# Kernel tuning notes

Measured on AMD Instinct MI355X. Metric: run time of the kernel, lower is better.

Reference implementation:

```python
import jax, jax.numpy as jnp
import numpy as np

B, L, D, E, H = 4, 2048, 512, 8, 1024

def setup_inputs() -> dict:
    key = jax.random.key(0)
    k1, k2, k3, k4 = jax.random.split(key, 4)
    x = jax.random.normal(k1, (B, L, D), dtype=jnp.float32)
    weights = jax.random.uniform(k2, (B, L, E), dtype=jnp.float32)
    w1 = jax.random.normal(k3, (E, D, H), dtype=jnp.float32) * 0.02
    b1 = jnp.zeros((E, H), dtype=jnp.float32)
    w2 = jax.random.normal(k4, (E, H, D), dtype=jnp.float32) * 0.02
    b2 = jnp.zeros((E, D), dtype=jnp.float32)
    return {"x": x, "weights": weights, "w1": w1, "b1": b1, "w2": w2, "b2": b2}

def reference(x, weights, w1, b1, w2, b2):
    # h: [B, L, E, H]
    h = jnp.einsum('bld,edh->bleh', x, w1) + b1[None, None, :, :]
    h = jax.nn.gelu(h, approximate=False)  # torch F.gelu default is exact (erf)
    # out: [B, L, E, D]
    out = jnp.einsum('bleh,ehd->bled', h, w2) + b2[None, None, :, :]
    # weighted sum over experts -> [B, L, D]
    return jnp.einsum('bled,ble->bld', out, weights)
```

## Files before the change

kernel.cpp:

```cpp
#include <hip/hip_runtime.h>
#include <hip/hip_bf16.h>

#define DEV __device__ __forceinline__

typedef __bf16 bf16;
typedef __bf16 bf16x4 __attribute__((ext_vector_type(4)));
typedef __bf16 bf16x8 __attribute__((ext_vector_type(8)));
typedef float f32x4 __attribute__((ext_vector_type(4)));

static constexpr int Bb = 4, Ll = 2048, Dd = 512, Ee = 8, Hh = 1024;
static constexpr int Mm = Bb * Ll;
static constexpr int GKS = Ee * Hh;
static constexpr int TSZ = 65536;

DEV void gload_lds16(const void* g, void* l) {
  __builtin_amdgcn_global_load_lds(
      (const __attribute__((address_space(1))) unsigned int*)g,
      (__attribute__((address_space(3))) unsigned int*)l, 16, 0, 0);
}

DEV float gelu_fast(float h) {
  const float k = 0.7978845608028654f * 2.0f * 1.4426950408889634f;
  float h2 = h * h;
  float y = h * (k + (0.044715f * k) * h2);
  float t = exp2f(y);
  return h - h * __frcp_rn(t + 1.0f);
}

__global__ void cvt_x_kernel(const float* __restrict__ in, bf16* __restrict__ out, int n4) {
  int i = blockIdx.x * blockDim.x + threadIdx.x;
  if (i < n4) {
    float4 v = ((const float4*)in)[i];
    bf16x4 o = {(bf16)v.x, (bf16)v.y, (bf16)v.z, (bf16)v.w};
    ((bf16x4*)out)[i] = o;
  }
}

__global__ void transpose_cvt(const float* __restrict__ in, bf16* __restrict__ out,
                              int R, int C, size_t in_es, size_t out_es, int out_rs) {
  __shared__ float tile[64][65];
  const int e = blockIdx.z;
  const float* ip = in + (size_t)e * in_es;
  bf16* op = out + (size_t)e * out_es;
  const int r0 = blockIdx.y * 64, c0 = blockIdx.x * 64;
  const int tc = threadIdx.x & 63, tr = threadIdx.x >> 6;
#pragma unroll
  for (int i = 0; i < 16; ++i) {
    const int r = tr + i * 4;
    tile[r][tc] = ip[(size_t)(r0 + r) * C + c0 + tc];
  }
  __syncthreads();
  const int wr = threadIdx.x & 63, wc0 = threadIdx.x >> 6;
#pragma unroll
  for (int i = 0; i < 16; ++i) {
    const int c = wc0 + i * 4;
    op[(size_t)(c0 + c) * out_rs + r0 + wr] = (bf16)tile[wr][c];
  }
}

#define PIPE_DECLS                                                   \
  const int t = threadIdx.x;                                         \
  const int lane = t & 63;                                           \
  const int wid = t >> 6;                                            \
  const int wm = wid >> 2, wn = wid & 3;                             \
  const int fr = lane & 15, fg = lane >> 4, fq = lane >> 4;          \
  const int srow = t >> 2;                                           \
  const int sq = (t & 3) ^ ((t >> 3) & 3);                           \
  const int rsl = fg ^ ((fr >> 1) & 3);

#define PHASE0(buf)                                                  \
  bf16x8 bfr[4], af[4];                                              \
  _Pragma("unroll") for (int fj = 0; fj < 4; ++fj) {                 \
    const int row = wn * 64 + fj * 16 + fr;                          \
    bfr[fj] = *(const bf16x8*)((buf) + 16384 + row * 64 + rsl * 16); \
  }                                                                  \
  _Pragma("unroll") for (int fi = 0; fi < 4; ++fi) {                 \
    const int row = wm * 128 + fi * 16 + fr;                         \
    af[fi] = *(const bf16x8*)((buf) + row * 64 + rsl * 16);          \
  }

#define PHASE1_READS(buf)                                            \
  bf16x8 af2[4];                                                     \
  _Pragma("unroll") for (int fi = 0; fi < 4; ++fi) {                 \
    const int row = wm * 128 + (4 + fi) * 16 + fr;                   \
    af2[fi] = *(const bf16x8*)((buf) + row * 64 + rsl * 16);         \
  }

#define MFMA_CLUSTER(A, ACCOFF)                                      \
  __builtin_amdgcn_s_barrier();                                      \
  asm volatile("s_waitcnt lgkmcnt(0)" ::: "memory");                 \
  __builtin_amdgcn_sched_barrier(0);                                 \
  __builtin_amdgcn_s_setprio(1);                                     \
  _Pragma("unroll") for (int fi = 0; fi < 4; ++fi)                   \
  _Pragma("unroll") for (int fj = 0; fj < 4; ++fj)                   \
    acc[(ACCOFF) + fi][fj] = __builtin_amdgcn_mfma_f32_16x16x32_bf16(\
        bfr[fj], (A)[fi], acc[(ACCOFF) + fi][fj], 0, 0, 0);          \
  __builtin_amdgcn_s_setprio(0);

__global__ __launch_bounds__(512, 1) void ffn_stage1_f(
    const bf16* __restrict__ xb, const bf16* __restrict__ w1t,
    const float* __restrict__ b1, const float* __restrict__ wts,
    bf16* __restrict__ G) {
  __shared__ __align__(16) char lds[98304];
  __shared__ float b1s[1024];
  __shared__ float wls[256];
  const int mt = blockIdx.x, e = blockIdx.y;
  PIPE_DECLS
  b1s[t] = b1[e * Hh + t];
  b1s[512 + t] = b1[e * Hh + 512 + t];
  if (t < 256) wls[t] = wts[((size_t)mt * 256 + t) * Ee + e];

  const bf16* Ag = xb + (size_t)mt * 256 * Dd;
  const bf16* Bg0 = w1t + (size_t)e * Hh * Dd;

  auto stageA = [&](int it, char* buf) {
    const int k0 = (it & 15) * 32;
    gload_lds16(Ag + (size_t)srow * Dd + k0 + sq * 8, buf + wid * 1024);
    gload_lds16(Ag + (size_t)(128 + srow) * Dd + k0 + sq * 8, buf + 8192 + wid * 1024);
  };
  auto stageB = [&](int it, char* buf) {
    const bf16* Bg = Bg0 + (size_t)(it >> 4) * 256 * Dd;
    const int k0 = (it & 15) * 32;
    gload_lds16(Bg + (size_t)srow * Dd + k0 + sq * 8, buf + 16384 + wid * 1024);
    gload_lds16(Bg + (size_t)(128 + srow) * Dd + k0 + sq * 8, buf + 24576 + wid * 1024);
  };

  f32x4 acc[8][4] = {};
  const int NT = 64;
  stageA(0, lds); stageB(0, lds);
  stageA(1, lds + 32768); stageB(1, lds + 32768);
  for (int it = 0; it < NT; ++it) {
    char* buf = lds + (it % 3) * 32768;
    char* nbuf = lds + ((it + 2) % 3) * 32768;
    if (it + 1 < NT) {
      asm volatile("s_waitcnt vmcnt(4)" ::: "memory");
    } else {
      asm volatile("s_waitcnt vmcnt(0)" ::: "memory");
    }
    __builtin_amdgcn_s_barrier();
    {
      PHASE0(buf)
      if (it + 2 < NT) stageA(it + 2, nbuf);
      MFMA_CLUSTER(af, 0)
      PHASE1_READS(buf)
      if (it + 2 < NT) stageB(it + 2, nbuf);
      MFMA_CLUSTER(af2, 4)
    }
    if ((it & 15) == 15) {
      const int ct = it >> 4;
      bf16* tbase = G + ((((size_t)e * 32 + mt) * 4) + ct) * TSZ;
      float b1v[4][4];
#pragma unroll
      for (int fj = 0; fj < 4; ++fj)
#pragma unroll
        for (int r = 0; r < 4; ++r)
          b1v[fj][r] = b1s[ct * 256 + wn * 64 + fj * 16 + fq * 4 + r];
#pragma unroll
      for (int fi = 0; fi < 8; ++fi) {
        const int mp = wm * 128 + fi * 16 + fr;
        const float wgt = wls[mp];
        bf16* gp = tbase + (size_t)mp * 256 + wn * 64 + fq * 4;
#pragma unroll
        for (int fj = 0; fj < 4; ++fj) {
          bf16x4 o;
#pragma unroll
          for (int r = 0; r < 4; ++r) {
            float v = acc[fi][fj][r] + b1v[fj][r];
            o[r] = (bf16)(gelu_fast(v) * wgt);
          }
          __builtin_nontemporal_store(o, (bf16x4*)(gp + fj * 16));
#pragma unroll
          for (int r = 0; r < 4; ++r) acc[fi][fj][r] = 0.f;
        }
      }
    }
  }
}

__global__ __launch_bounds__(512, 1) void ffn_stage2_f(
    const bf16* __restrict__ G, const bf16* __restrict__ w2t,
    float* __restrict__ P, int eslabs) {
  __shared__ __align__(16) char lds[98304];
  const int mt = blockIdx.x, nt = blockIdx.y, s = blockIdx.z;
  PIPE_DECLS
  const bf16* Bg = w2t + (size_t)nt * 256 * GKS + (size_t)s * eslabs * Hh;

  auto stageA = [&](int it, char* buf) {
    const int eidx = s * eslabs + (it >> 5);
    const int ct = (it >> 3) & 3;
    const int hp = (it & 7) * 32;
    const bf16* tb = G + ((((size_t)eidx * 32 + mt) * 4) + ct) * TSZ;
    gload_lds16(tb + (size_t)srow * 256 + hp + sq * 8, buf + wid * 1024);
    gload_lds16(tb + (size_t)(128 + srow) * 256 + hp + sq * 8, buf + 8192 + wid * 1024);
  };
  auto stageB = [&](int it, char* buf) {
    const int k0 = it * 32;
    gload_lds16(Bg + (size_t)srow * GKS + k0 + sq * 8, buf + 16384 + wid * 1024);
    gload_lds16(Bg + (size_t)(128 + srow) * GKS + k0 + sq * 8, buf + 24576 + wid * 1024);
  };

  f32x4 acc[8][4] = {};
  const int NT = eslabs * 32;
  stageA(0, lds); stageB(0, lds);
  stageA(1, lds + 32768); stageB(1, lds + 32768);
  for (int it = 0; it < NT; ++it) {
    char* buf = lds + (it % 3) * 32768;
    char* nbuf = lds + ((it + 2) % 3) * 32768;
    if (it + 1 < NT) {
      asm volatile("s_waitcnt vmcnt(4)" ::: "memory");
    } else {
      asm volatile("s_waitcnt vmcnt(0)" ::: "memory");
    }
    __builtin_amdgcn_s_barrier();
    {
      PHASE0(buf)
      if (it + 2 < NT) stageA(it + 2, nbuf);
      MFMA_CLUSTER(af, 0)
      PHASE1_READS(buf)
      if (it + 2 < NT) stageB(it + 2, nbuf);
      MFMA_CLUSTER(af2, 4)
    }
  }

  float* Pp = P + (size_t)s * Mm * Dd;
#pragma unroll
  for (int fi = 0; fi < 8; ++fi) {
    const size_t m = (size_t)mt * 256 + wm * 128 + fi * 16 + fr;
    float* pp = Pp + m * Dd + nt * 256 + wn * 64 + fq * 4;
#pragma unroll
    for (int fj = 0; fj < 4; ++fj)
      __builtin_nontemporal_store(acc[fi][fj], (f32x4*)(pp + fj * 16));
  }
}

__global__ __launch_bounds__(256) void reduce_bias(
    const float* __restrict__ P, const float* __restrict__ wts,
    const float* __restrict__ b2, float* __restrict__ out, int S) {
  const int n4 = Mm * Dd / 4;
  int i = blockIdx.x * 256 + threadIdx.x;
  if (i >= n4) return;
  const int m = i / (Dd / 4);
  const int d0 = (i % (Dd / 4)) * 4;
  f32x4 a = __builtin_nontemporal_load((const f32x4*)P + i);
  for (int s = 1; s < S; ++s) {
    f32x4 p = __builtin_nontemporal_load((const f32x4*)P + (size_t)s * n4 + i);
    a += p;
  }
  const float* wr = wts + (size_t)m * Ee;
#pragma unroll
  for (int e = 0; e < Ee; ++e) {
    const float w = wr[e];
    const float* b = b2 + e * Dd + d0;
    a[0] += w * b[0]; a[1] += w * b[1]; a[2] += w * b[2]; a[3] += w * b[3];
  }
  ((f32x4*)out)[i] = a;
}

extern "C" void kernel_launch(void* const* d_in, const int* in_sizes, int n_in,
                              void* d_out, int out_size, void* d_ws, size_t ws_size,
                              hipStream_t stream) {
  const float* x   = (const float*)d_in[0];
  const float* wts = (const float*)d_in[1];
  const float* w1  = (const float*)d_in[2];
  const float* b1  = (const float*)d_in[3];
  const float* w2  = (const float*)d_in[4];
  const float* b2  = (const float*)d_in[5];
  float* out = (float*)d_out;

  char* ws = (char*)d_ws;
  size_t off = 0;
  bf16* xb  = (bf16*)(ws + off); off += (size_t)Mm * Dd * 2;
  bf16* w1t = (bf16*)(ws + off); off += (size_t)Ee * Hh * Dd * 2;
  bf16* w2t = (bf16*)(ws + off); off += (size_t)Dd * Ee * Hh * 2;

  const size_t gfull = (size_t)Mm * Ee * Hh * 2;
  const size_t psz   = (size_t)Mm * Dd * 4;

  cvt_x_kernel<<<(Mm * Dd / 4 + 255) / 256, 256, 0, stream>>>(x, xb, Mm * Dd / 4);
  transpose_cvt<<<dim3(Hh / 64, Dd / 64, Ee), 256, 0, stream>>>(
      w1, w1t, Dd, Hh, (size_t)Dd * Hh, (size_t)Hh * Dd, Dd);
  transpose_cvt<<<dim3(Dd / 64, Hh / 64, Ee), 256, 0, stream>>>(
      w2, w2t, Hh, Dd, (size_t)Hh * Dd, (size_t)Hh, Ee * Hh);

  int S = 0;
  if (ws_size >= off + gfull + 4 * psz) S = 4;
  else if (ws_size >= off + gfull + 2 * psz) S = 2;

  if (S >= 2) {
    bf16* G = (bf16*)(ws + off);
    float* P = (float*)(ws + off + gfull);
    ffn_stage1_f<<<dim3(Mm / 256, Ee), 512, 0, stream>>>(
        xb, w1t, b1, wts, G);
    ffn_stage2_f<<<dim3(Mm / 256, Dd / 256, S), 512, 0, stream>>>(
        G, w2t, P, Ee / S);
    reduce_bias<<<(Mm * Dd / 4 + 255) / 256, 256, 0, stream>>>(P, wts, b2, out, S);
  }
}
```

Before: 253.1 us.

## Store stage-2 partial sums in bf16, vectorize transpose loads, drop nontemporal stores

The split-K partial sums written by stage 2 and read by the reduction kernel change from fp32 to bf16. This halves the traffic of that intermediate buffer, at the cost of extra rounding error in the partials before they are summed in fp32. The weight transpose kernel now reads float4 vectors instead of scalars. The nontemporal hints on the G and P stores are replaced with plain stores, so the intermediates may stay in cache for the next kernel.

```diff
diff --git a/kernel.cpp b/kernel.cpp
--- a/kernel.cpp
+++ b/kernel.cpp
@@ -43,11 +43,13 @@
   const float* ip = in + (size_t)e * in_es;
   bf16* op = out + (size_t)e * out_es;
   const int r0 = blockIdx.y * 64, c0 = blockIdx.x * 64;
-  const int tc = threadIdx.x & 63, tr = threadIdx.x >> 6;
-#pragma unroll
-  for (int i = 0; i < 16; ++i) {
-    const int r = tr + i * 4;
-    tile[r][tc] = ip[(size_t)(r0 + r) * C + c0 + tc];
+  const int rr = threadIdx.x >> 4, c4 = (threadIdx.x & 15) * 4;
+#pragma unroll
+  for (int i = 0; i < 4; ++i) {
+    const int r = rr + i * 16;
+    float4 v = *(const float4*)(ip + (size_t)(r0 + r) * C + c0 + c4);
+    tile[r][c4] = v.x; tile[r][c4 + 1] = v.y;
+    tile[r][c4 + 2] = v.z; tile[r][c4 + 3] = v.w;
   }
   __syncthreads();
   const int wr = threadIdx.x & 63, wc0 = threadIdx.x >> 6;
@@ -168,7 +170,7 @@
             float v = acc[fi][fj][r] + b1v[fj][r];
             o[r] = (bf16)(gelu_fast(v) * wgt);
           }
-          __builtin_nontemporal_store(o, (bf16x4*)(gp + fj * 16));
+          *(bf16x4*)(gp + fj * 16) = o;
 #pragma unroll
           for (int r = 0; r < 4; ++r) acc[fi][fj][r] = 0.f;
         }
@@ -179,7 +181,7 @@
 
 __global__ __launch_bounds__(512, 1) void ffn_stage2_f(
     const bf16* __restrict__ G, const bf16* __restrict__ w2t,
-    float* __restrict__ P, int eslabs) {
+    bf16* __restrict__ P, int eslabs) {
   __shared__ __align__(16) char lds[98304];
   const int mt = blockIdx.x, nt = blockIdx.y, s = blockIdx.z;
   PIPE_DECLS
@@ -222,29 +224,34 @@
     }
   }
 
-  float* Pp = P + (size_t)s * Mm * Dd;
+  bf16* Pp = P + (size_t)s * Mm * Dd;
 #pragma unroll
   for (int fi = 0; fi < 8; ++fi) {
     const size_t m = (size_t)mt * 256 + wm * 128 + fi * 16 + fr;
-    float* pp = Pp + m * Dd + nt * 256 + wn * 64 + fq * 4;
-#pragma unroll
-    for (int fj = 0; fj < 4; ++fj)
-      __builtin_nontemporal_store(acc[fi][fj], (f32x4*)(pp + fj * 16));
-  }
-}
-
+    bf16* pp = Pp + m * Dd + nt * 256 + wn * 64 + fq * 4;
+#pragma unroll
+    for (int fj = 0; fj < 4; ++fj) {
+      bf16x4 o = {(bf16)acc[fi][fj][0], (bf16)acc[fi][fj][1],
+                  (bf16)acc[fi][fj][2], (bf16)acc[fi][fj][3]};
+      *(bf16x4*)(pp + fj * 16) = o;
+    }
+  }
+}
+
+typedef short short4v __attribute__((ext_vector_type(4)));
 __global__ __launch_bounds__(256) void reduce_bias(
-    const float* __restrict__ P, const float* __restrict__ wts,
+    const bf16* __restrict__ P, const float* __restrict__ wts,
     const float* __restrict__ b2, float* __restrict__ out, int S) {
   const int n4 = Mm * Dd / 4;
   int i = blockIdx.x * 256 + threadIdx.x;
   if (i >= n4) return;
   const int m = i / (Dd / 4);
   const int d0 = (i % (Dd / 4)) * 4;
-  f32x4 a = __builtin_nontemporal_load((const f32x4*)P + i);
-  for (int s = 1; s < S; ++s) {
-    f32x4 p = __builtin_nontemporal_load((const f32x4*)P + (size_t)s * n4 + i);
-    a += p;
+  f32x4 a = {0.f, 0.f, 0.f, 0.f};
+  for (int s = 0; s < S; ++s) {
+    bf16x4 p = ((const bf16x4*)P)[(size_t)s * n4 + i];
+#pragma unroll
+    for (int r = 0; r < 4; ++r) a[r] += (float)p[r];
   }
   const float* wr = wts + (size_t)m * Ee;
 #pragma unroll
@@ -274,7 +281,7 @@
   bf16* w2t = (bf16*)(ws + off); off += (size_t)Dd * Ee * Hh * 2;
 
   const size_t gfull = (size_t)Mm * Ee * Hh * 2;
-  const size_t psz   = (size_t)Mm * Dd * 4;
+  const size_t psz   = (size_t)Mm * Dd * 2;
 
   cvt_x_kernel<<<(Mm * Dd / 4 + 255) / 256, 256, 0, stream>>>(x, xb, Mm * Dd / 4);
   transpose_cvt<<<dim3(Hh / 64, Dd / 64, Ee), 256, 0, stream>>>(
@@ -288,7 +295,7 @@
 
   if (S >= 2) {
     bf16* G = (bf16*)(ws + off);
-    float* P = (float*)(ws + off + gfull);
+    bf16* P = (bf16*)(ws + off + gfull);
     ffn_stage1_f<<<dim3(Mm / 256, Ee), 512, 0, stream>>>(
         xb, w1t, b1, wts, G);
     ffn_stage2_f<<<dim3(Mm / 256, Dd / 256, S), 512, 0, stream>>>(
```

After: 215.3 us. -14.9%, faster.
